# Kernel tuning notes

Measured on AMD Instinct MI355X. Metric: run time of the kernel, lower is better.

The kernel has to match this reference:

```python
import jax, jax.numpy as jnp
import numpy as np

B, N, K, NC, EMB, Z, AD = 16, 2048, 20, 16, 1024, 256, 64

def _lrelu(x):
    return jnp.where(x > 0, x, 0.2 * x)

def _bn(x, g, b, axes):
    # BatchNorm (training-mode batch stats, biased var, eps=1e-5); channel axis = 1
    m = x.mean(axes, keepdims=True)
    v = x.var(axes, keepdims=True)
    sh = [1] * x.ndim; sh[1] = -1
    return (x - m) * jax.lax.rsqrt(v + 1e-5) * g.reshape(sh) + b.reshape(sh)

def _c2(w, x):  # 1x1 Conv2d, no bias
    return jnp.einsum('oc,bcnk->bonk', w, x)

def _c1(w, x):  # 1x1 Conv1d, no bias
    return jnp.einsum('oc,bcn->bon', w, x)

def _knn(x, k):  # x: (B,C,N) -> idx (B,N,k)
    inner = -2.0 * jnp.einsum('bcn,bcm->bnm', x, x)
    xx = jnp.sum(x * x, axis=1)  # (B,N)
    pd = -xx[:, :, None] - inner - xx[:, None, :]  # negative squared dist
    return jax.lax.top_k(pd, k)[1]

def _graph_feat(x, idx):  # x: (B,C,N), idx: (B,N,k) -> (B,2C,N,k)
    xt = x.transpose(0, 2, 1)  # (B,N,C)
    feat = jax.vmap(lambda a, i: a[i])(xt, idx)  # (B,N,k,C)
    xc = jnp.broadcast_to(xt[:, :, None, :], feat.shape)
    return jnp.concatenate([feat - xc, xc], axis=-1).transpose(0, 3, 1, 2)

def setup_inputs():
    key = jax.random.key(0)
    ks = jax.random.split(key, 16)
    rn = lambda k, sh: (jax.random.normal(k, sh) * 0.05).astype(jnp.float32)
    d = {
        'xyz': jax.random.normal(ks[0], (B, N, 3), jnp.float32),
        'flow': jax.random.normal(ks[1], (B, N, 3), jnp.float32),
        'eps': jax.random.normal(ks[2], (B, Z), jnp.float32),
        'w_c1a': rn(ks[3], (60, 6)),   'w_c1b': rn(ks[4], (60, 60)),
        'w_c2a': rn(ks[5], (60, 120)), 'w_c2b': rn(ks[6], (60, 60)),
        'w_c3': rn(ks[7], (EMB, 120)),
        'w_mu': rn(ks[8], (Z, EMB)),  'b_mu': jnp.zeros((Z,), jnp.float32),
        'w_var': rn(ks[9], (Z, EMB)), 'b_var': jnp.zeros((Z,), jnp.float32),
        'w_enc': rn(ks[10], (64, NC)),
        'w_cub1': rn(ks[11], (256, Z + 64)), 'w_cub2': rn(ks[12], (120, 256)),
        'w_q': rn(ks[13], (AD, 120)), 'w_k': rn(ks[14], (AD, 120)),
    }
    for nm, c in [('c1a', 60), ('c1b', 60), ('c2a', 60), ('c2b', 60), ('c3', EMB)]:
        d['g_' + nm] = jnp.ones((c,), jnp.float32)
        d['bb_' + nm] = jnp.zeros((c,), jnp.float32)
    return d

def reference(xyz, flow, eps, w_c1a, w_c1b, w_c2a, w_c2b, w_c3, w_mu, b_mu,
              w_var, b_var, w_enc, w_cub1, w_cub2, w_q, w_k,
              g_c1a, bb_c1a, g_c1b, bb_c1b, g_c2a, bb_c2a, g_c2b, bb_c2b, g_c3, bb_c3):
    x = xyz.transpose(0, 2, 1)  # (B,3,N)
    idx = _knn(x, K)
    h = _graph_feat(x, idx)  # (B,6,N,K)
    h = _lrelu(_bn(_c2(w_c1a, h), g_c1a, bb_c1a, (0, 2, 3)))
    h = _lrelu(_bn(_c2(w_c1b, h), g_c1b, bb_c1b, (0, 2, 3)))
    x1 = h.max(axis=-1)  # (B,60,N)
    h = _graph_feat(x1, idx)  # low_dim_idx=1: reuse xyz knn
    h = _lrelu(_bn(_c2(w_c2a, h), g_c2a, bb_c2a, (0, 2, 3)))
    h = _lrelu(_bn(_c2(w_c2b, h), g_c2b, bb_c2b, (0, 2, 3)))
    x2 = h.max(axis=-1)
    x_per = jnp.concatenate([x1, x2], axis=1)  # (B,120,N)
    g = _lrelu(_bn(_c1(w_c3, x_per), g_c3, bb_c3, (0, 2))).max(axis=-1)  # (B,EMB)
    mu = g @ w_mu.T + b_mu
    log_var = g @ w_var.T + b_var
    z = eps * jnp.exp(0.5 * log_var) + mu  # (B,Z)
    cub = jnp.broadcast_to(jnp.eye(NC, dtype=xyz.dtype), (xyz.shape[0], NC, NC))
    cvec = _lrelu(_c1(w_enc, cub))  # (B,64,NC)
    xc = jnp.concatenate([jnp.broadcast_to(z[:, :, None], (z.shape[0], Z, NC)), cvec], axis=1)
    xc = _lrelu(_c1(w_cub1, xc))
    x_cuboid = _lrelu(_c1(w_cub2, xc))  # (B,120,NC)
    Q = _c1(w_q, x_per) / jnp.sqrt(jnp.float32(AD))  # (B,AD,N)
    Kf = _c1(w_k, x_cuboid)  # (B,AD,NC)
    scores = jnp.einsum('bcm,bcn->bmn', Kf, Q)  # (B,NC,N)
    assign = jax.nn.softmax(scores, axis=1).transpose(0, 2, 1)  # (B,N,NC)
    return (x_per, x_cuboid, z[:, :, None], mu, log_var, assign)
```

## Files before the change

### kernel.cpp

```cpp
#include <hip/hip_runtime.h>

typedef unsigned int u32;
typedef unsigned short u16;

#define BB 16
#define NN 2048
#define KK 20
#define EE (BB*NN*KK)
#define PP (BB*NN)
#define NCHK 8
#define CHKSZ (NN/NCHK)

#define O_XPER 0
#define O_XCUB 3932160
#define O_Z    3962880
#define O_MU   3966976
#define O_LV   3971072
#define O_ASG  3975168

__device__ double g_part[4096*128];
__device__ double g_std[2560];
__device__ float  g_st[2560];
__device__ float  g_gsf[BB*1024];
__device__ float  g_zf[BB*256];
__device__ float  g_Kf[BB*1024];
__device__ u16    g_idx[EE];
__device__ float  g_xpf[(size_t)PP*120];
__device__ float  g_e1[(size_t)EE*60];
__device__ float  g_e2[(size_t)EE*60];

#define S1A_D 0
#define S1B_D 128
#define S2A_D 256
#define S2B_D 384
#define S3S_D 512
#define S3Q_D 1536
#define S1A_AB 0
#define S1B_AB 128
#define S2A_AB 256
#define S2B_AB 384
#define S3A 512
#define S3B 1536

#define NEG_BIG -1.0e30f

__device__ __forceinline__ float lrelu(float x){ return x > 0.f ? x : 0.2f*x; }

__device__ __forceinline__ void xrow(int bn, int c0, int cnt, float* d){
  const float* s = g_xpf + (size_t)bn*120 + c0;
  #pragma unroll 4
  for (int i=0;i<cnt;i+=4){
    float4 v = *(const float4*)(s+i);
    d[i]=v.x; d[i+1]=v.y; d[i+2]=v.z; d[i+3]=v.w;
  }
}

__device__ __forceinline__ float pdcalc(float4 pm, float qx, float qy, float qz, float qw){
  float dot = fmaf(qx,pm.x, fmaf(qy,pm.y, qz*pm.z));
  float t = fmaf(2.f, dot, -qw);
  return t - pm.w;
}

#define KT_DECL \
  float td0=NEG_BIG,td1=NEG_BIG,td2=NEG_BIG,td3=NEG_BIG,td4=NEG_BIG, \
        td5=NEG_BIG,td6=NEG_BIG,td7=NEG_BIG,td8=NEG_BIG,td9=NEG_BIG, \
        td10=NEG_BIG,td11=NEG_BIG,td12=NEG_BIG,td13=NEG_BIG,td14=NEG_BIG, \
        td15=NEG_BIG,td16=NEG_BIG,td17=NEG_BIG,td18=NEG_BIG,td19=NEG_BIG;
#define KT_CSW(u,l) { float mx = fmaxf(td##u, td##l); float mn = fminf(td##u, td##l); td##u = mx; td##l = mn; }
#define KT_INSERT(pd) \
  if ((pd) > td19){ \
    td19 = (pd); \
    KT_CSW(18,19) KT_CSW(17,18) KT_CSW(16,17) KT_CSW(15,16) \
    KT_CSW(14,15) KT_CSW(13,14) KT_CSW(12,13) KT_CSW(11,12) \
    KT_CSW(10,11) KT_CSW(9,10)  KT_CSW(8,9)   KT_CSW(7,8)   \
    KT_CSW(6,7)   KT_CSW(5,6)   KT_CSW(4,5)   KT_CSW(3,4)   \
    KT_CSW(2,3)   KT_CSW(1,2)   KT_CSW(0,1) }

__global__ __launch_bounds__(128) void k_knnt(const float* __restrict__ xyz){
  __shared__ float4 cand[CHKSZ];
  int qg = blockIdx.x >> 3;
  int c  = blockIdx.x & 7;
  int b  = qg >> 4;
  int n0 = (qg & 15) << 7;
  int t  = threadIdx.x;
  int m0 = c*CHKSZ;
  for (int i=t;i<CHKSZ;i+=128){
    const float* s = xyz + ((size_t)((b<<11)+m0+i))*3;
    float x=s[0], y=s[1], z=s[2];
    cand[i] = make_float4(x,y,z, fmaf(x,x,fmaf(y,y,z*z)));
  }
  __syncthreads();
  int n = n0 + t;
  const float* qs = xyz + ((size_t)((b<<11)+n))*3;
  float qx=qs[0], qy=qs[1], qz=qs[2];
  float qw = fmaf(qx,qx,fmaf(qy,qy,qz*qz));
  KT_DECL
  for (int i=0;i<CHKSZ;i++){
    float pd = pdcalc(cand[i], qx,qy,qz,qw);
    KT_INSERT(pd)
  }
  int p = (b<<11) + n;
  float* outd = g_e1;
  #define KOUT(k) outd[(size_t)(c*KK+k)*PP + p] = td##k;
  KOUT(0) KOUT(1) KOUT(2) KOUT(3) KOUT(4) KOUT(5) KOUT(6) KOUT(7) KOUT(8) KOUT(9)
  KOUT(10) KOUT(11) KOUT(12) KOUT(13) KOUT(14) KOUT(15) KOUT(16) KOUT(17) KOUT(18) KOUT(19)
  #undef KOUT
}

__global__ __launch_bounds__(256) void k_knnu(){
  int q = blockIdx.x*256 + threadIdx.x;
  const float* ind = g_e1;
  KT_DECL
  for (int i=0;i<NCHK*KK;i++){
    float pd = ind[(size_t)i*PP + q];
    KT_INSERT(pd)
  }
  g_e2[q] = td19;
}

__global__ __launch_bounds__(256) void k_knns1(const float* __restrict__ xyz){
  __shared__ float4 cand[CHKSZ];
  int gid = blockIdx.x*256 + threadIdx.x;
  int c = gid >> 15;
  int q = gid & (PP-1);
  int b = q >> 11;
  int t = threadIdx.x;
  for (int i=t;i<CHKSZ;i+=256){
    const float* s = xyz + ((size_t)((b<<11)+c*CHKSZ+i))*3;
    float x=s[0], y=s[1], z=s[2];
    cand[i] = make_float4(x,y,z, fmaf(x,x,fmaf(y,y,z*z)));
  }
  __syncthreads();
  const float* qs = xyz + (size_t)q*3;
  float qx=qs[0], qy=qs[1], qz=qs[2];
  float qw = fmaf(qx,qx,fmaf(qy,qy,qz*qz));
  float T = g_e2[q];
  u32 cgt=0, ceq=0;
  for (int i=0;i<CHKSZ;i++){
    float pd = pdcalc(cand[i], qx,qy,qz,qw);
    cgt += (pd > T) ? 1u : 0u;
    ceq += (pd == T) ? 1u : 0u;
  }
  u32* cntg = (u32*)g_part;
  u32* cnte = cntg + NCHK*PP;
  cntg[c*PP + q] = cgt;
  cnte[c*PP + q] = ceq;
}

__global__ __launch_bounds__(256) void k_knns2(){
  int q = blockIdx.x*256 + threadIdx.x;
  u32* cntg = (u32*)g_part;
  u32* cnte = cntg + NCHK*PP;
  u32* bg   = cnte + NCHK*PP;
  u32* be   = bg   + NCHK*PP;
  u32 acc = 0;
  for (int c=0;c<NCHK;c++){ bg[c*PP+q] = acc; acc += cntg[c*PP+q]; }
  u32 eacc = acc;
  for (int c=0;c<NCHK;c++){ be[c*PP+q] = eacc; eacc += cnte[c*PP+q]; }
}

__global__ __launch_bounds__(256) void k_knns3(const float* __restrict__ xyz){
  __shared__ float4 cand[CHKSZ];
  int gid = blockIdx.x*256 + threadIdx.x;
  int c = gid >> 15;
  int q = gid & (PP-1);
  int b = q >> 11;
  int t = threadIdx.x;
  for (int i=t;i<CHKSZ;i+=256){
    const float* s = xyz + ((size_t)((b<<11)+c*CHKSZ+i))*3;
    float x=s[0], y=s[1], z=s[2];
    cand[i] = make_float4(x,y,z, fmaf(x,x,fmaf(y,y,z*z)));
  }
  __syncthreads();
  const float* qs = xyz + (size_t)q*3;
  float qx=qs[0], qy=qs[1], qz=qs[2];
  float qw = fmaf(qx,qx,fmaf(qy,qy,qz*qz));
  float T = g_e2[q];
  const u32* cntg = (const u32*)g_part;
  const u32* cnte = cntg + NCHK*PP;
  const u32* bg   = cnte + NCHK*PP;
  const u32* be   = bg   + NCHK*PP;
  u32 wgt = bg[c*PP+q];
  u32 weq = be[c*PP+q];
  u16* o = g_idx + (size_t)q*KK;
  for (int i=0;i<CHKSZ;i++){
    float pd = pdcalc(cand[i], qx,qy,qz,qw);
    int m = c*CHKSZ + i;
    if (pd > T && wgt < KK){ o[wgt] = (u16)m; wgt++; }
    else if (pd == T && weq < KK){ o[weq] = (u16)m; weq++; }
  }
}

__global__ __launch_bounds__(256) void k_red60(int dbase, int nblk){
  __shared__ double red[256];
  int s = blockIdx.x;
  int t = threadIdx.x;
  double acc = 0.0;
  for (int i=t;i<nblk;i+=256) acc += g_part[(size_t)i*128 + s];
  red[t] = acc; __syncthreads();
  for (int w=128; w>0; w>>=1){ if (t<w) red[t]+=red[t+w]; __syncthreads(); }
  if (t==0) g_std[dbase+s] = red[0];
}

__global__ __launch_bounds__(64) void k_fin(const float* __restrict__ g, const float* __restrict__ bb,
                                            int dbase, int abase, double invc){
  int c = threadIdx.x;
  if (c < 60){
    double m = g_std[dbase+c]*invc;
    double v = g_std[dbase+64+c]*invc - m*m;
    if (v < 0.0) v = 0.0;
    float r = (float)(1.0/sqrt(v + 1e-5));
    float a = r*g[c];
    g_st[abase+c] = a;
    g_st[abase+64+c] = bb[c] - (float)m*a;
  }
}
__global__ __launch_bounds__(64) void k_fin3(const float* __restrict__ g, const float* __restrict__ bb, double invc){
  int c = blockIdx.x*64 + threadIdx.x;
  double m = g_std[S3S_D+c]*invc;
  double v = g_std[S3Q_D+c]*invc - m*m;
  if (v < 0.0) v = 0.0;
  float r = (float)(1.0/sqrt(v + 1e-5));
  float a = r*g[c];
  g_st[S3A+c] = a;
  g_st[S3B+c] = bb[c] - (float)m*a;
}

__global__ __launch_bounds__(256) void k_conv1a(const float* __restrict__ xyz, const float* __restrict__ w1a){
  __shared__ float ws[360];
  __shared__ double sred[512];
  int tid = threadIdx.x, lane = tid & 63, wv = tid >> 6;
  for (int i=tid;i<360;i+=256) ws[i]=w1a[i];
  __syncthreads();
  int edge = blockIdx.x*256 + tid;
  int row = edge / KK;
  int b = row >> 11;
  int nbr = g_idx[edge];
  const float* cp = xyz + (size_t)row*3;
  const float* np2 = xyz + ((size_t)((b<<11)+nbr))*3;
  float c0=cp[0], c1=cp[1], c2=cp[2];
  float d0=np2[0]-c0, d1=np2[1]-c1, d2=np2[2]-c2;
  double rs=0.0, rq=0.0;
  for (int o=0;o<60;o++){
    float y = ws[o*6]*d0 + ws[o*6+1]*d1 + ws[o*6+2]*d2 + ws[o*6+3]*c0 + ws[o*6+4]*c1 + ws[o*6+5]*c2;
    g_e1[(size_t)o*EE + edge] = y;
    float s=y, q=y*y;
    #pragma unroll
    for (int m=1;m<64;m<<=1){ s += __shfl_xor(s,m); q += __shfl_xor(q,m); }
    if (lane==o){ rs += (double)s; rq += (double)q; }
  }
  sred[wv*128 + lane] = rs;
  sred[wv*128 + 64 + lane] = rq;
  __syncthreads();
  if (tid < 128)
    g_part[(size_t)blockIdx.x*128 + tid] = sred[tid] + sred[128+tid] + sred[256+tid] + sred[384+tid];
}

__global__ __launch_bounds__(256) void k_conv1b(const float* __restrict__ w1b){
  __shared__ float wbs[3600];
  __shared__ float As[60], Bs[60];
  __shared__ double sred[512];
  int tid = threadIdx.x, lane = tid & 63, wv = tid >> 6;
  for (int i=tid;i<3600;i+=256) wbs[i]=w1b[i];
  if (tid<60){ As[tid]=g_st[S1A_AB+tid]; Bs[tid]=g_st[S1A_AB+64+tid]; }
  __syncthreads();
  int edge = blockIdx.x*256 + tid;
  float h[60];
  #pragma unroll 4
  for (int o=0;o<60;o++) h[o] = lrelu(fmaf(As[o], g_e1[(size_t)o*EE + edge], Bs[o]));
  double rs=0.0, rq=0.0;
  for (int o=0;o<60;o++){
    float y=0.f;
    #pragma unroll
    for (int c=0;c<60;c++) y = fmaf(wbs[o*60+c], h[c], y);
    g_e2[(size_t)o*EE + edge] = y;
    float s=y, q=y*y;
    #pragma unroll
    for (int m=1;m<64;m<<=1){ s += __shfl_xor(s,m); q += __shfl_xor(q,m); }
    if (lane==o){ rs += (double)s; rq += (double)q; }
  }
  sred[wv*128 + lane] = rs;
  sred[wv*128 + 64 + lane] = rq;
  __syncthreads();
  if (tid < 128)
    g_part[(size_t)blockIdx.x*128 + tid] = sred[tid] + sred[128+tid] + sred[256+tid] + sred[384+tid];
}

__global__ __launch_bounds__(256) void k_final1s(float* __restrict__ outb){
  int o = blockIdx.x >> 7;
  int bn = ((blockIdx.x & 127) << 8) + threadIdx.x;
  int b = bn >> 11, n = bn & 2047;
  float A = g_st[S1B_AB+o], Bv = g_st[S1B_AB+64+o];
  const float* src = g_e2 + (size_t)o*EE + (size_t)bn*KK;
  float mx = NEG_BIG;
  #pragma unroll
  for (int k=0;k<KK;k++) mx = fmaxf(mx, lrelu(fmaf(A, src[k], Bv)));
  g_xpf[(size_t)bn*120 + o] = mx;
  outb[O_XPER + (size_t)(b*120+o)*NN + n] = mx;
}

__global__ __launch_bounds__(256) void k_pgem2(const float* __restrict__ w2a){
  __shared__ float wd[3600], wcd[3600];
  int tid = threadIdx.x;
  for (int i=tid;i<3600;i+=256){
    int o = i/60, c = i%60;
    float a = w2a[o*120+c], bvl = w2a[o*120+60+c];
    wd[i] = a; wcd[i] = bvl - a;
  }
  __syncthreads();
  int p = blockIdx.x*256 + tid;
  float x[60];
  xrow(p, 0, 60, x);
  float* gU = g_e2;
  float* gV = g_e2 + (size_t)PP*64;
  #pragma unroll 4
  for (int o=0;o<60;o++){
    float u=0.f, v=0.f;
    #pragma unroll
    for (int c=0;c<60;c++){ u = fmaf(wd[o*60+c], x[c], u); v = fmaf(wcd[o*60+c], x[c], v); }
    gU[(size_t)p*64 + o] = u;
    gV[(size_t)p*64 + o] = v;
  }
}

__global__ __launch_bounds__(256) void k_conv2a(){
  __shared__ double sred[512];
  int tid = threadIdx.x, lane = tid & 63, wv = tid >> 6;
  int edge = blockIdx.x*256 + tid;
  int row = edge / KK;
  int b = row >> 11;
  int nbr = g_idx[edge];
  int pn = (b<<11)+nbr;
  const float4* gU = (const float4*)g_e2;
  const float4* gV = (const float4*)(g_e2 + (size_t)PP*64);
  double rs=0.0, rq=0.0;
  #pragma unroll
  for (int o4=0;o4<15;o4++){
    float4 uu = gU[(size_t)pn*16 + o4];
    float4 vv = gV[(size_t)row*16 + o4];
    float y0=uu.x+vv.x, y1=uu.y+vv.y, y2=uu.z+vv.z, y3=uu.w+vv.w;
    g_e1[(size_t)(o4*4+0)*EE + edge] = y0;
    g_e1[(size_t)(o4*4+1)*EE + edge] = y1;
    g_e1[(size_t)(o4*4+2)*EE + edge] = y2;
    g_e1[(size_t)(o4*4+3)*EE + edge] = y3;
    float ys[4] = {y0,y1,y2,y3};
    #pragma unroll
    for (int j=0;j<4;j++){
      float s=ys[j], q=ys[j]*ys[j];
      #pragma unroll
      for (int m=1;m<64;m<<=1){ s += __shfl_xor(s,m); q += __shfl_xor(q,m); }
      if (lane==o4*4+j){ rs += (double)s; rq += (double)q; }
    }
  }
  sred[wv*128 + lane] = rs;
  sred[wv*128 + 64 + lane] = rq;
  __syncthreads();
  if (tid < 128)
    g_part[(size_t)blockIdx.x*128 + tid] = sred[tid] + sred[128+tid] + sred[256+tid] + sred[384+tid];
}

__global__ __launch_bounds__(256) void k_conv2b(const float* __restrict__ w2b){
  __shared__ float wbs[3600];
  __shared__ float As[60], Bs[60];
  __shared__ double sred[512];
  int tid = threadIdx.x, lane = tid & 63, wv = tid >> 6;
  for (int i=tid;i<3600;i+=256) wbs[i]=w2b[i];
  if (tid<60){ As[tid]=g_st[S2A_AB+tid]; Bs[tid]=g_st[S2A_AB+64+tid]; }
  __syncthreads();
  int edge = blockIdx.x*256 + tid;
  float h[60];
  #pragma unroll 4
  for (int o=0;o<60;o++) h[o] = lrelu(fmaf(As[o], g_e1[(size_t)o*EE + edge], Bs[o]));
  double rs=0.0, rq=0.0;
  for (int o=0;o<60;o++){
    float y=0.f;
    #pragma unroll
    for (int c=0;c<60;c++) y = fmaf(wbs[o*60+c], h[c], y);
    g_e2[(size_t)o*EE + edge] = y;
    float s=y, q=y*y;
    #pragma unroll
    for (int m=1;m<64;m<<=1){ s += __shfl_xor(s,m); q += __shfl_xor(q,m); }
    if (lane==o){ rs += (double)s; rq += (double)q; }
  }
  sred[wv*128 + lane] = rs;
  sred[wv*128 + 64 + lane] = rq;
  __syncthreads();
  if (tid < 128)
    g_part[(size_t)blockIdx.x*128 + tid] = sred[tid] + sred[128+tid] + sred[256+tid] + sred[384+tid];
}

__global__ __launch_bounds__(256) void k_final2s(float* __restrict__ outb){
  int o = blockIdx.x >> 7;
  int bn = ((blockIdx.x & 127) << 8) + threadIdx.x;
  int b = bn >> 11, n = bn & 2047;
  float A = g_st[S2B_AB+o], Bv = g_st[S2B_AB+64+o];
  const float* src = g_e2 + (size_t)o*EE + (size_t)bn*KK;
  float mx = NEG_BIG;
  #pragma unroll
  for (int k=0;k<KK;k++) mx = fmaxf(mx, lrelu(fmaf(A, src[k], Bv)));
  g_xpf[(size_t)bn*120 + 60 + o] = mx;
  outb[O_XPER + (size_t)(b*120+60+o)*NN + n] = mx;
}

__global__ __launch_bounds__(256) void k_conv3(const float* __restrict__ wc3){
  __shared__ float ws[64*120];
  __shared__ double sred[512];
  int tid = threadIdx.x, lane = tid & 63, wv = tid >> 6;
  int ec = blockIdx.x >> 7;
  int p = ((blockIdx.x & 127) << 8) + tid;
  const float* wsrc = wc3 + (size_t)ec*64*120;
  for (int i=tid;i<7680;i+=256) ws[i]=wsrc[i];
  __syncthreads();
  float x[120];
  xrow(p, 0, 120, x);
  double rs=0.0, rq=0.0;
  for (int ei=0; ei<64; ei++){
    float y=0.f;
    #pragma unroll
    for (int c=0;c<120;c++) y = fmaf(ws[ei*120+c], x[c], y);
    g_e1[(size_t)(ec*64+ei)*PP + p] = y;
    float s=y, q=y*y;
    #pragma unroll
    for (int m=1;m<64;m<<=1){ s += __shfl_xor(s,m); q += __shfl_xor(q,m); }
    if (lane==ei){ rs += (double)s; rq += (double)q; }
  }
  sred[wv*128 + lane] = rs;
  sred[wv*128 + 64 + lane] = rq;
  __syncthreads();
  if (tid < 128)
    g_part[(size_t)blockIdx.x*128 + tid] = sred[tid] + sred[128+tid] + sred[256+tid] + sred[384+tid];
}

__global__ __launch_bounds__(256) void k_red3(){
  __shared__ double reds[256], redq[256];
  int e = blockIdx.x;
  int ec = e >> 6, ei = e & 63;
  int t = threadIdx.x;
  double accs=0.0, accq=0.0;
  for (int pg=t; pg<128; pg+=256){
    size_t base = (size_t)(ec*128+pg)*128;
    accs += g_part[base + ei];
    accq += g_part[base + 64 + ei];
  }
  reds[t]=accs; redq[t]=accq; __syncthreads();
  for (int w=128; w>0; w>>=1){ if (t<w){ reds[t]+=reds[t+w]; redq[t]+=redq[t+w]; } __syncthreads(); }
  if (t==0){ g_std[S3S_D+e]=reds[0]; g_std[S3Q_D+e]=redq[0]; }
}

__global__ __launch_bounds__(256) void k_max3s(){
  __shared__ float red[256];
  int e = blockIdx.x >> 4;
  int b = blockIdx.x & 15;
  int t = threadIdx.x;
  float A = g_st[S3A+e], Bv = g_st[S3B+e];
  const float* src = g_e1 + (size_t)e*PP + b*NN;
  float mx = NEG_BIG;
  for (int i=t;i<NN;i+=256) mx = fmaxf(mx, lrelu(fmaf(A, src[i], Bv)));
  red[t]=mx; __syncthreads();
  for (int w=128;w>0;w>>=1){ if (t<w) red[t]=fmaxf(red[t],red[t+w]); __syncthreads(); }
  if (t==0) g_gsf[b*1024+e] = red[0];
}

__global__ __launch_bounds__(256) void k_head(const float* __restrict__ eps,
                                              const float* __restrict__ wmu, const float* __restrict__ bmu,
                                              const float* __restrict__ wvar, const float* __restrict__ bvar,
                                              float* __restrict__ outb){
  int b = blockIdx.x, j = threadIdx.x;
  __shared__ float gs[1024];
  for (int i=j;i<1024;i+=256) gs[i] = g_gsf[b*1024+i];
  __syncthreads();
  float mu = bmu[j], lv = bvar[j];
  const float4* wm = (const float4*)(wmu + (size_t)j*1024);
  const float4* wv = (const float4*)(wvar + (size_t)j*1024);
  #pragma unroll 4
  for (int e=0;e<256;e++){
    float4 a = wm[e], c = wv[e];
    const float* g4 = gs + e*4;
    mu = fmaf(a.x,g4[0], fmaf(a.y,g4[1], fmaf(a.z,g4[2], fmaf(a.w,g4[3], mu))));
    lv = fmaf(c.x,g4[0], fmaf(c.y,g4[1], fmaf(c.z,g4[2], fmaf(c.w,g4[3], lv))));
  }
  float z = fmaf(eps[b*256+j], expf(0.5f*lv), mu);
  g_zf[b*256+j] = z;
  outb[O_MU + b*256 + j] = mu;
  outb[O_LV + b*256 + j] = lv;
  outb[O_Z  + b*256 + j] = z;
}

__global__ __launch_bounds__(256) void k_cuboid(const float* __restrict__ wenc,
                                                const float* __restrict__ wcub1, const float* __restrict__ wcub2,
                                                const float* __restrict__ wk, float* __restrict__ outb){
  int b = blockIdx.x, t = threadIdx.x;
  __shared__ float xc[320*16];
  __shared__ float hh[256*16];
  __shared__ float xq[120*16];
  for (int i=t;i<320*16;i+=256){
    int c = i>>4, m = i&15;
    xc[i] = (c<256) ? g_zf[b*256+c] : lrelu(wenc[(c-256)*16+m]);
  }
  __syncthreads();
  {
    float acc[16];
    #pragma unroll
    for (int m=0;m<16;m++) acc[m]=0.f;
    for (int c=0;c<320;c++){
      float wv = wcub1[(size_t)t*320+c];
      #pragma unroll
      for (int m=0;m<16;m++) acc[m] = fmaf(wv, xc[c*16+m], acc[m]);
    }
    #pragma unroll
    for (int m=0;m<16;m++) hh[t*16+m] = lrelu(acc[m]);
  }
  __syncthreads();
  if (t<120){
    float a2[16];
    #pragma unroll
    for (int m=0;m<16;m++) a2[m]=0.f;
    for (int c=0;c<256;c++){
      float wv = wcub2[(size_t)t*256+c];
      #pragma unroll
      for (int m=0;m<16;m++) a2[m] = fmaf(wv, hh[c*16+m], a2[m]);
    }
    #pragma unroll
    for (int m=0;m<16;m++){
      float v = lrelu(a2[m]);
      xq[t*16+m] = v;
      outb[O_XCUB + b*1920 + t*16 + m] = v;
    }
  }
  __syncthreads();
  if (t<64){
    float a3[16];
    #pragma unroll
    for (int m=0;m<16;m++) a3[m]=0.f;
    for (int c=0;c<120;c++){
      float wv = wk[t*120+c];
      #pragma unroll
      for (int m=0;m<16;m++) a3[m] = fmaf(wv, xq[c*16+m], a3[m]);
    }
    #pragma unroll
    for (int m=0;m<16;m++) g_Kf[b*1024 + t*16 + m] = a3[m];
  }
}

__global__ __launch_bounds__(64) void k_attn(const float* __restrict__ wq, float* __restrict__ outb){
  int p = blockIdx.x*64 + threadIdx.x;
  int b = p >> 11;
  float x[120];
  xrow(p, 0, 120, x);
  float sc[16];
  #pragma unroll
  for (int m=0;m<16;m++) sc[m]=0.f;
  for (int a=0;a<64;a++){
    float q=0.f;
    #pragma unroll
    for (int c=0;c<120;c++) q = fmaf(wq[a*120+c], x[c], q);
    q *= 0.125f;
    const float* kf = g_Kf + b*1024 + a*16;
    #pragma unroll
    for (int m=0;m<16;m++) sc[m] = fmaf(kf[m], q, sc[m]);
  }
  float mx = sc[0];
  #pragma unroll
  for (int m=1;m<16;m++) mx = fmaxf(mx, sc[m]);
  float s=0.f;
  #pragma unroll
  for (int m=0;m<16;m++){ sc[m] = expf(sc[m]-mx); s += sc[m]; }
  float inv = 1.f/s;
  #pragma unroll
  for (int m=0;m<16;m++) outb[O_ASG + (size_t)p*16 + m] = sc[m]*inv;
}

extern "C" void kernel_launch(void* const* d_in, const int* in_sizes, int n_in,
                              void* d_out, int out_size, void* d_ws, size_t ws_size,
                              hipStream_t stream){
  const float* xyz  = (const float*)d_in[0];
  const float* eps  = (const float*)d_in[2];
  const float* w1a  = (const float*)d_in[3];
  const float* w1b  = (const float*)d_in[4];
  const float* w2a  = (const float*)d_in[5];
  const float* w2b  = (const float*)d_in[6];
  const float* wc3  = (const float*)d_in[7];
  const float* wmu  = (const float*)d_in[8];
  const float* bmu  = (const float*)d_in[9];
  const float* wvar = (const float*)d_in[10];
  const float* bvar = (const float*)d_in[11];
  const float* wenc = (const float*)d_in[12];
  const float* wcub1= (const float*)d_in[13];
  const float* wcub2= (const float*)d_in[14];
  const float* wq   = (const float*)d_in[15];
  const float* wk   = (const float*)d_in[16];
  const float* g1a  = (const float*)d_in[17];
  const float* b1a  = (const float*)d_in[18];
  const float* g1b  = (const float*)d_in[19];
  const float* b1b  = (const float*)d_in[20];
  const float* g2a  = (const float*)d_in[21];
  const float* b2a  = (const float*)d_in[22];
  const float* g2b  = (const float*)d_in[23];
  const float* b2b  = (const float*)d_in[24];
  const float* g3   = (const float*)d_in[25];
  const float* b3   = (const float*)d_in[26];
  float* outb = (float*)d_out;

  const double inv1 = 1.0/(double)EE;
  const double inv3 = 1.0/(double)PP;

  k_knnt<<<2048,128,0,stream>>>(xyz);
  k_knnu<<<128,256,0,stream>>>();
  k_knns1<<<1024,256,0,stream>>>(xyz);
  k_knns2<<<128,256,0,stream>>>();
  k_knns3<<<1024,256,0,stream>>>(xyz);
  k_conv1a<<<2560,256,0,stream>>>(xyz, w1a);
  k_red60<<<128,256,0,stream>>>(S1A_D, 2560);
  k_fin<<<1,64,0,stream>>>(g1a, b1a, S1A_D, S1A_AB, inv1);
  k_conv1b<<<2560,256,0,stream>>>(w1b);
  k_red60<<<128,256,0,stream>>>(S1B_D, 2560);
  k_fin<<<1,64,0,stream>>>(g1b, b1b, S1B_D, S1B_AB, inv1);
  k_final1s<<<7680,256,0,stream>>>(outb);
  k_pgem2<<<128,256,0,stream>>>(w2a);
  k_conv2a<<<2560,256,0,stream>>>();
  k_red60<<<128,256,0,stream>>>(S2A_D, 2560);
  k_fin<<<1,64,0,stream>>>(g2a, b2a, S2A_D, S2A_AB, inv1);
  k_conv2b<<<2560,256,0,stream>>>(w2b);
  k_red60<<<128,256,0,stream>>>(S2B_D, 2560);
  k_fin<<<1,64,0,stream>>>(g2b, b2b, S2B_D, S2B_AB, inv1);
  k_final2s<<<7680,256,0,stream>>>(outb);
  k_conv3<<<2048,256,0,stream>>>(wc3);
  k_red3<<<1024,256,0,stream>>>();
  k_fin3<<<16,64,0,stream>>>(g3, b3, inv3);
  k_max3s<<<16384,256,0,stream>>>();
  k_head<<<16,256,0,stream>>>(eps, wmu, bmu, wvar, bvar, outb);
  k_cuboid<<<16,256,0,stream>>>(wenc, wcub1, wcub2, wk, outb);
  k_attn<<<512,64,0,stream>>>(wq, outb);
}
```

Measured before the change: 1.504 ms.

## Compute BN stats of linear convs via input Gram matrices and skip materialization

For conv1a and conv3, whose inputs feed straight into a linear 1x1 conv, the batch-norm mean and variance are now taken from the input's first and second moments (a Gram matrix) projected through the weights. The conv outputs are no longer written to global memory. conv1a is recomputed inside conv1b, and conv3 becomes a fused tile-based kernel that tracks a per-channel max and min of the pre-BN value. The sign of the BN scale then picks which one passes through the monotone affine plus leaky-ReLU. This removes large global writes and reads of the EMB×N activation and the edge-level e1 tensor. In exchange it adds extra Gram kernels and relies on double-precision moment accumulation for numerical accuracy.

New measurement: 1.648 ms. 1.1x slower.

```diff
diff --git a/kernel.cpp b/kernel.cpp
--- a/kernel.cpp
+++ b/kernel.cpp
@@ -18,10 +18,9 @@
 #define O_LV   3971072
 #define O_ASG  3975168
 
-__device__ double g_part[4096*128];
+__device__ double g_part[524288];
 __device__ double g_std[2560];
 __device__ float  g_st[2560];
-__device__ float  g_gsf[BB*1024];
 __device__ float  g_zf[BB*256];
 __device__ float  g_Kf[BB*1024];
 __device__ u16    g_idx[EE];
@@ -29,18 +28,19 @@
 __device__ float  g_e1[(size_t)EE*60];
 __device__ float  g_e2[(size_t)EE*60];
 
-#define S1A_D 0
 #define S1B_D 128
 #define S2A_D 256
 #define S2B_D 384
-#define S3S_D 512
-#define S3Q_D 1536
 #define S1A_AB 0
 #define S1B_AB 128
 #define S2A_AB 256
 #define S2B_AB 384
 #define S3A 512
 #define S3B 1536
+
+#define G3_OFF 300000
+#define XS_OFF 314400
+#define MB_OFF 320000
 
 #define NEG_BIG -1.0e30f
 
@@ -215,22 +215,89 @@
     g_st[abase+64+c] = bb[c] - (float)m*a;
   }
 }
-__global__ __launch_bounds__(64) void k_fin3(const float* __restrict__ g, const float* __restrict__ bb, double invc){
-  int c = blockIdx.x*64 + threadIdx.x;
-  double m = g_std[S3S_D+c]*invc;
-  double v = g_std[S3Q_D+c]*invc - m*m;
-  if (v < 0.0) v = 0.0;
-  float r = (float)(1.0/sqrt(v + 1e-5));
-  float a = r*g[c];
-  g_st[S3A+c] = a;
-  g_st[S3B+c] = bb[c] - (float)m*a;
-}
-
-__global__ __launch_bounds__(256) void k_conv1a(const float* __restrict__ xyz, const float* __restrict__ w1a){
+
+__global__ __launch_bounds__(256) void k_gram1(const float* __restrict__ xyz){
+  __shared__ double sred[128];
+  int tid = threadIdx.x, lane = tid & 63, wv = tid >> 6;
+  double acc[27];
+  #pragma unroll
+  for (int k=0;k<27;k++) acc[k]=0.0;
+  for (int it=0; it<8; ++it){
+    int edge = (it*320 + blockIdx.x)*256 + tid;
+    int row = edge / KK;
+    int b = row >> 11;
+    int nbr = g_idx[edge];
+    const float* cp = xyz + (size_t)row*3;
+    const float* np2 = xyz + ((size_t)((b<<11)+nbr))*3;
+    float f3=cp[0], f4=cp[1], f5=cp[2];
+    float f0=np2[0]-f3, f1=np2[1]-f4, f2=np2[2]-f5;
+    float f[6] = {f0,f1,f2,f3,f4,f5};
+    #pragma unroll
+    for (int i=0;i<6;i++) acc[i] += (double)f[i];
+    int k=6;
+    #pragma unroll
+    for (int i=0;i<6;i++)
+      #pragma unroll
+      for (int j=i;j<6;j++){ acc[k] += (double)f[i]*(double)f[j]; k++; }
+  }
+  #pragma unroll
+  for (int k=0;k<27;k++){
+    double s = acc[k];
+    #pragma unroll
+    for (int m=1;m<64;m<<=1) s += __shfl_xor(s,m);
+    if (lane==0) sred[wv*32+k] = s;
+  }
+  __syncthreads();
+  if (tid < 27)
+    g_part[(size_t)blockIdx.x*32 + tid] = sred[tid] + sred[32+tid] + sred[64+tid] + sred[96+tid];
+}
+
+__global__ __launch_bounds__(64) void k_fing1(const float* __restrict__ w1a,
+                                              const float* __restrict__ gg, const float* __restrict__ bb){
+  __shared__ double gsum[27];
+  int t = threadIdx.x;
+  if (t < 27){
+    double s = 0.0;
+    for (int i=0;i<320;i++) s += g_part[(size_t)i*32 + t];
+    gsum[t] = s;
+  }
+  __syncthreads();
+  if (t < 60){
+    float w[6];
+    #pragma unroll
+    for (int i=0;i<6;i++) w[i] = w1a[t*6+i];
+    double S = 0.0;
+    #pragma unroll
+    for (int i=0;i<6;i++) S += (double)w[i]*gsum[i];
+    double Q = 0.0; int k = 6;
+    #pragma unroll
+    for (int i=0;i<6;i++)
+      #pragma unroll
+      for (int j=i;j<6;j++){
+        double cf = (i==j) ? 1.0 : 2.0;
+        Q += cf*(double)w[i]*(double)w[j]*gsum[k]; k++;
+      }
+    double inv1 = 1.0/(double)EE;
+    double m = S*inv1;
+    double v = Q*inv1 - m*m;
+    if (v < 0.0) v = 0.0;
+    float r = (float)(1.0/sqrt(v + 1e-5));
+    float A = r*gg[t];
+    g_st[S1A_AB+t] = A;
+    g_st[S1A_AB+64+t] = bb[t] - (float)m*A;
+  }
+}
+
+__global__ __launch_bounds__(256) void k_conv1b(const float* __restrict__ xyz,
+                                                const float* __restrict__ w1a, const float* __restrict__ w1b){
   __shared__ float ws[360];
+  __shared__ float wbs[3600];
+  __shared__ float As[60], Bs[60];
   __shared__ double sred[512];
   int tid = threadIdx.x, lane = tid & 63, wv = tid >> 6;
   for (int i=tid;i<360;i+=256) ws[i]=w1a[i];
+  for (int i=tid;i<3600;i+=256) wbs[i]=w1b[i];
+  if (tid<60){ As[tid]=g_st[S1A_AB+tid]; Bs[tid]=g_st[S1A_AB+64+tid]; }
   __syncthreads();
   int edge = blockIdx.x*256 + tid;
   int row = edge / KK;
@@ -240,34 +307,12 @@
   const float* np2 = xyz + ((size_t)((b<<11)+nbr))*3;
   float c0=cp[0], c1=cp[1], c2=cp[2];
   float d0=np2[0]-c0, d1=np2[1]-c1, d2=np2[2]-c2;
-  double rs=0.0, rq=0.0;
+  float h[60];
+  #pragma unroll 4
   for (int o=0;o<60;o++){
     float y = ws[o*6]*d0 + ws[o*6+1]*d1 + ws[o*6+2]*d2 + ws[o*6+3]*c0 + ws[o*6+4]*c1 + ws[o*6+5]*c2;
-    g_e1[(size_t)o*EE + edge] = y;
-    float s=y, q=y*y;
-    #pragma unroll
-    for (int m=1;m<64;m<<=1){ s += __shfl_xor(s,m); q += __shfl_xor(q,m); }
-    if (lane==o){ rs += (double)s; rq += (double)q; }
-  }
-  sred[wv*128 + lane] = rs;
-  sred[wv*128 + 64 + lane] = rq;
-  __syncthreads();
-  if (tid < 128)
-    g_part[(size_t)blockIdx.x*128 + tid] = sred[tid] + sred[128+tid] + sred[256+tid] + sred[384+tid];
-}
-
-__global__ __launch_bounds__(256) void k_conv1b(const float* __restrict__ w1b){
-  __shared__ float wbs[3600];
-  __shared__ float As[60], Bs[60];
-  __shared__ double sred[512];
-  int tid = threadIdx.x, lane = tid & 63, wv = tid >> 6;
-  for (int i=tid;i<3600;i+=256) wbs[i]=w1b[i];
-  if (tid<60){ As[tid]=g_st[S1A_AB+tid]; Bs[tid]=g_st[S1A_AB+64+tid]; }
-  __syncthreads();
-  int edge = blockIdx.x*256 + tid;
-  float h[60];
-  #pragma unroll 4
-  for (int o=0;o<60;o++) h[o] = lrelu(fmaf(As[o], g_e1[(size_t)o*EE + edge], Bs[o]));
+    h[o] = lrelu(fmaf(As[o], y, Bs[o]));
+  }
   double rs=0.0, rq=0.0;
   for (int o=0;o<60;o++){
     float y=0.f;
@@ -402,63 +447,128 @@
   outb[O_XPER + (size_t)(b*120+60+o)*NN + n] = mx;
 }
 
-__global__ __launch_bounds__(256) void k_conv3(const float* __restrict__ wc3){
-  __shared__ float ws[64*120];
-  __shared__ double sred[512];
-  int tid = threadIdx.x, lane = tid & 63, wv = tid >> 6;
-  int ec = blockIdx.x >> 7;
-  int p = ((blockIdx.x & 127) << 8) + tid;
-  const float* wsrc = wc3 + (size_t)ec*64*120;
-  for (int i=tid;i<7680;i+=256) ws[i]=wsrc[i];
-  __syncthreads();
-  float x[120];
-  xrow(p, 0, 120, x);
-  double rs=0.0, rq=0.0;
-  for (int ei=0; ei<64; ei++){
-    float y=0.f;
-    #pragma unroll
-    for (int c=0;c<120;c++) y = fmaf(ws[ei*120+c], x[c], y);
-    g_e1[(size_t)(ec*64+ei)*PP + p] = y;
-    float s=y, q=y*y;
-    #pragma unroll
-    for (int m=1;m<64;m<<=1){ s += __shfl_xor(s,m); q += __shfl_xor(q,m); }
-    if (lane==ei){ rs += (double)s; rq += (double)q; }
-  }
-  sred[wv*128 + lane] = rs;
-  sred[wv*128 + 64 + lane] = rq;
-  __syncthreads();
-  if (tid < 128)
-    g_part[(size_t)blockIdx.x*128 + tid] = sred[tid] + sred[128+tid] + sred[256+tid] + sred[384+tid];
-}
-
-__global__ __launch_bounds__(256) void k_red3(){
-  __shared__ double reds[256], redq[256];
-  int e = blockIdx.x;
-  int ec = e >> 6, ei = e & 63;
-  int t = threadIdx.x;
-  double accs=0.0, accq=0.0;
-  for (int pg=t; pg<128; pg+=256){
-    size_t base = (size_t)(ec*128+pg)*128;
-    accs += g_part[base + ei];
-    accq += g_part[base + 64 + ei];
-  }
-  reds[t]=accs; redq[t]=accq; __syncthreads();
-  for (int w=128; w>0; w>>=1){ if (t<w){ reds[t]+=reds[t+w]; redq[t]+=redq[t+w]; } __syncthreads(); }
-  if (t==0){ g_std[S3S_D+e]=reds[0]; g_std[S3Q_D+e]=redq[0]; }
-}
-
-__global__ __launch_bounds__(256) void k_max3s(){
-  __shared__ float red[256];
-  int e = blockIdx.x >> 4;
-  int b = blockIdx.x & 15;
-  int t = threadIdx.x;
-  float A = g_st[S3A+e], Bv = g_st[S3B+e];
-  const float* src = g_e1 + (size_t)e*PP + b*NN;
-  float mx = NEG_BIG;
-  for (int i=t;i<NN;i+=256) mx = fmaxf(mx, lrelu(fmaf(A, src[i], Bv)));
-  red[t]=mx; __syncthreads();
-  for (int w=128;w>0;w>>=1){ if (t<w) red[t]=fmaxf(red[t],red[t+w]); __syncthreads(); }
-  if (t==0) g_gsf[b*1024+e] = red[0];
+__global__ __launch_bounds__(256) void k_gram3(){
+  __shared__ float xt[64*120];
+  int tid = threadIdx.x;
+  int il = tid>>6, jl = tid&63;
+  int iblk = blockIdx.x>>4, pc = blockIdx.x&15;
+  int i = iblk*4 + il;
+  double a0=0.0, a1=0.0, asum=0.0;
+  for (int tile=0; tile<32; tile++){
+    int p0 = pc*2048 + tile*64;
+    __syncthreads();
+    for (int v=tid; v<1920; v+=256){
+      int pk = v/30, c4 = v%30;
+      ((float4*)xt)[pk*30+c4] = *(const float4*)(g_xpf + (size_t)(p0+pk)*120 + c4*4);
+    }
+    __syncthreads();
+    for (int k=0;k<64;k++){
+      float xi = xt[k*120 + i];
+      a0 += (double)xi*(double)xt[k*120 + jl];
+      if (jl < 56) a1 += (double)xi*(double)xt[k*120 + 64 + jl];
+      if (jl == 0) asum += (double)xi;
+    }
+  }
+  g_part[(size_t)blockIdx.x*512 + il*120 + jl] = a0;
+  if (jl < 56) g_part[(size_t)blockIdx.x*512 + il*120 + 64 + jl] = a1;
+  if (jl == 0) g_part[(size_t)blockIdx.x*512 + 480 + il] = asum;
+}
+
+__global__ __launch_bounds__(256) void k_fing3r(){
+  int id = blockIdx.x*256 + threadIdx.x;
+  if (id < 14400){
+    int i = id/120, j = id%120;
+    int iblk = i>>2, slot = (i&3)*120 + j;
+    double s = 0.0;
+    for (int pc=0;pc<16;pc++) s += g_part[(size_t)(iblk*16+pc)*512 + slot];
+    g_part[G3_OFF + id] = s;
+  } else if (id < 14520){
+    int i = id - 14400;
+    int iblk = i>>2, slot = 480 + (i&3);
+    double s = 0.0;
+    for (int pc=0;pc<16;pc++) s += g_part[(size_t)(iblk*16+pc)*512 + slot];
+    g_part[XS_OFF + i] = s;
+  }
+}
+
+__global__ __launch_bounds__(64) void k_fin3G(const float* __restrict__ wc3,
+                                              const float* __restrict__ gg, const float* __restrict__ bb){
+  __shared__ float wsm[120];
+  int e = blockIdx.x, l = threadIdx.x;
+  for (int c=l;c<120;c+=64) wsm[c] = wc3[(size_t)e*120 + c];
+  __syncthreads();
+  double Q=0.0, S=0.0;
+  for (int id=l; id<14400; id+=64){
+    int i = id/120, j = id%120;
+    Q += (double)wsm[i]*(double)wsm[j]*g_part[G3_OFF + id];
+  }
+  for (int i=l;i<120;i+=64) S += (double)wsm[i]*g_part[XS_OFF + i];
+  #pragma unroll
+  for (int m=1;m<64;m<<=1){ Q += __shfl_xor(Q,m); S += __shfl_xor(S,m); }
+  if (l==0){
+    double inv3 = 1.0/(double)PP;
+    double mm = S*inv3;
+    double v = Q*inv3 - mm*mm;
+    if (v < 0.0) v = 0.0;
+    float r = (float)(1.0/sqrt(v + 1e-5));
+    float A = r*gg[e];
+    g_st[S3A+e] = A;
+    g_st[S3B+e] = bb[e] - (float)mm*A;
+  }
+}
+
+__global__ __launch_bounds__(256) void k_max3f(const float* __restrict__ wc3){
+  __shared__ float xt[64*120];
+  __shared__ float red[512];
+  int tid = threadIdx.x;
+  int pj = tid>>6, ei = tid&63;
+  int ec = blockIdx.x>>6;
+  int b  = (blockIdx.x>>2)&15;
+  int seg= blockIdx.x&3;
+  int e  = ec*64 + ei;
+  float w[120];
+  {
+    const float4* wp = (const float4*)(wc3 + (size_t)e*120);
+    #pragma unroll
+    for (int c4=0;c4<30;c4++){
+      float4 t = wp[c4];
+      w[c4*4]=t.x; w[c4*4+1]=t.y; w[c4*4+2]=t.z; w[c4*4+3]=t.w;
+    }
+  }
+  float mx = NEG_BIG, mn = -NEG_BIG;
+  for (int tile=0; tile<8; tile++){
+    int p0 = b*2048 + seg*512 + tile*64;
+    __syncthreads();
+    for (int v=tid; v<1920; v+=256){
+      int pk = v/30, c4 = v%30;
+      ((float4*)xt)[pk*30+c4] = *(const float4*)(g_xpf + (size_t)(p0+pk)*120 + c4*4);
+    }
+    __syncthreads();
+    for (int k=pj*16; k<pj*16+16; k++){
+      const float* xr = xt + k*120;
+      float a0=0.f,a1=0.f,a2=0.f,a3=0.f;
+      #pragma unroll
+      for (int c=0;c<120;c+=4){
+        a0 = fmaf(w[c],   xr[c],   a0);
+        a1 = fmaf(w[c+1], xr[c+1], a1);
+        a2 = fmaf(w[c+2], xr[c+2], a2);
+        a3 = fmaf(w[c+3], xr[c+3], a3);
+      }
+      float y = (a0+a1)+(a2+a3);
+      mx = fmaxf(mx, y);
+      mn = fminf(mn, y);
+    }
+  }
+  __syncthreads();
+  red[tid] = mx; red[256+tid] = mn;
+  __syncthreads();
+  if (pj==0){
+    float M  = fmaxf(fmaxf(red[ei],red[64+ei]), fmaxf(red[128+ei],red[192+ei]));
+    float m2 = fminf(fminf(red[256+ei],red[320+ei]), fminf(red[384+ei],red[448+ei]));
+    float* MB = (float*)(g_part + MB_OFF);
+    MB[(seg*16+b)*1024 + e] = M;
+    MB[65536 + (seg*16+b)*1024 + e] = m2;
+  }
 }
 
 __global__ __launch_bounds__(256) void k_head(const float* __restrict__ eps,
@@ -467,7 +577,18 @@
                                               float* __restrict__ outb){
   int b = blockIdx.x, j = threadIdx.x;
   __shared__ float gs[1024];
-  for (int i=j;i<1024;i+=256) gs[i] = g_gsf[b*1024+i];
+  const float* MB = (const float*)(g_part + MB_OFF);
+  for (int i=j;i<1024;i+=256){
+    float A = g_st[S3A+i], B = g_st[S3B+i];
+    float M = NEG_BIG, m2 = -NEG_BIG;
+    #pragma unroll
+    for (int sg=0;sg<4;sg++){
+      M  = fmaxf(M,  MB[(sg*16+b)*1024 + i]);
+      m2 = fminf(m2, MB[65536 + (sg*16+b)*1024 + i]);
+    }
+    float y = (A > 0.f) ? M : ((A < 0.f) ? m2 : M);
+    gs[i] = lrelu(fmaf(A, y, B));
+  }
   __syncthreads();
   float mu = bmu[j], lv = bvar[j];
   const float4* wm = (const float4*)(wmu + (size_t)j*1024);
@@ -602,17 +723,15 @@
   float* outb = (float*)d_out;
 
   const double inv1 = 1.0/(double)EE;
-  const double inv3 = 1.0/(double)PP;
 
   k_knnt<<<2048,128,0,stream>>>(xyz);
   k_knnu<<<128,256,0,stream>>>();
   k_knns1<<<1024,256,0,stream>>>(xyz);
   k_knns2<<<128,256,0,stream>>>();
   k_knns3<<<1024,256,0,stream>>>(xyz);
-  k_conv1a<<<2560,256,0,stream>>>(xyz, w1a);
-  k_red60<<<128,256,0,stream>>>(S1A_D, 2560);
-  k_fin<<<1,64,0,stream>>>(g1a, b1a, S1A_D, S1A_AB, inv1);
-  k_conv1b<<<2560,256,0,stream>>>(w1b);
+  k_gram1<<<320,256,0,stream>>>(xyz);
+  k_fing1<<<1,64,0,stream>>>(w1a, g1a, b1a);
+  k_conv1b<<<2560,256,0,stream>>>(xyz, w1a, w1b);
   k_red60<<<128,256,0,stream>>>(S1B_D, 2560);
   k_fin<<<1,64,0,stream>>>(g1b, b1b, S1B_D, S1B_AB, inv1);
   k_final1s<<<7680,256,0,stream>>>(outb);
@@ -624,10 +743,10 @@
   k_red60<<<128,256,0,stream>>>(S2B_D, 2560);
   k_fin<<<1,64,0,stream>>>(g2b, b2b, S2B_D, S2B_AB, inv1);
   k_final2s<<<7680,256,0,stream>>>(outb);
-  k_conv3<<<2048,256,0,stream>>>(wc3);
-  k_red3<<<1024,256,0,stream>>>();
-  k_fin3<<<16,64,0,stream>>>(g3, b3, inv3);
-  k_max3s<<<16384,256,0,stream>>>();
+  k_gram3<<<480,256,0,stream>>>();
+  k_fing3r<<<57,256,0,stream>>>();
+  k_fin3G<<<1024,64,0,stream>>>(wc3, g3, b3);
+  k_max3f<<<1024,256,0,stream>>>(wc3);
   k_head<<<16,256,0,stream>>>(eps, wmu, bmu, wvar, bvar, outb);
   k_cuboid<<<16,256,0,stream>>>(wenc, wcub1, wcub2, wk, outb);
   k_attn<<<512,64,0,stream>>>(wq, outb);
```
